# Optimization experiments

Hardware: AMD Instinct MI355X
Metric: run time of the kernel (lower is better)

Reference implementation:

```python
import jax, jax.numpy as jnp
from jax import lax
import numpy as np

DN = ('NCHW', 'OIHW', 'NCHW')
LEAKY_SLOPE = 0.01  # torch nn.LeakyReLU default


def conv(x, w, b=None, stride=1, pad=0):
    y = lax.conv_general_dilated(x, w, (stride, stride), [(pad, pad), (pad, pad)],
                                 dimension_numbers=DN)
    return y if b is None else y + b[None, :, None, None]


def conv_transpose2d(x, w, b):
    # torch ConvTranspose2d(k=4, s=2, p=1); w layout (Cin, Cout, 4, 4)
    wf = jnp.transpose(jnp.flip(w, (2, 3)), (1, 0, 2, 3))  # -> OIHW
    y = lax.conv_general_dilated(x, wf, (1, 1), [(2, 2), (2, 2)],
                                 lhs_dilation=(2, 2), dimension_numbers=DN)
    return y + b[None, :, None, None]


def residual_stack(x, rw3, rw1):
    # 6 ResidualLayers: x + conv1x1(relu(conv3x3(x))), both convs bias-free
    for i in range(rw3.shape[0]):
        h = jax.nn.relu(conv(x, rw3[i], pad=1))
        x = x + conv(h, rw1[i])
    return x


def vector_quantize(latents, codebook):
    # latents: [B, D, H, W] -> NHWC
    lat = jnp.transpose(latents, (0, 2, 3, 1))
    B, H, W, D = lat.shape
    flat = lat.reshape(-1, D)  # [N, D]
    # pairwise squared distances [N, K]
    dist = (jnp.sum(flat ** 2, axis=1, keepdims=True)
            + jnp.sum(codebook ** 2, axis=1)
            - 2.0 * flat @ codebook.T)
    inds = jnp.argmin(dist, axis=1)            # [N]
    q = codebook[inds].reshape(B, H, W, D)     # gather == one-hot matmul
    commitment_loss = jnp.mean((lax.stop_gradient(q) - lat) ** 2)
    embedding_loss = jnp.mean((q - lax.stop_gradient(lat)) ** 2)
    q_st = lat + lax.stop_gradient(q - lat)    # straight-through
    return jnp.transpose(q_st, (0, 3, 1, 2)), embedding_loss, commitment_loss


def setup_inputs() -> dict:
    key = jax.random.key(0)
    ks = iter(jax.random.split(key, 32))
    B, C, S = 16, 3, 128
    H0, H1 = 128, 256          # hidden_dims
    D, K = 64, 512             # embedding_dim, num_embeddings
    n_res = 6

    def w(shape, scale=0.05):
        return (jax.random.normal(next(ks), shape, dtype=jnp.float32) * scale)

    inp = {
        'x': jax.random.normal(next(ks), (B, C, S, S), dtype=jnp.float32),
        # encoder
        'ew0': w((H0, C, 4, 4)), 'eb0': jnp.zeros((H0,), jnp.float32),
        'ew1': w((H1, H0, 4, 4)), 'eb1': jnp.zeros((H1,), jnp.float32),
        'ew2': w((H1, H1, 3, 3)), 'eb2': jnp.zeros((H1,), jnp.float32),
        'erw3': w((n_res, H1, H1, 3, 3)),
        'erw1': w((n_res, H1, H1, 1, 1)),
        'ew3': w((D, H1, 1, 1)), 'eb3': jnp.zeros((D,), jnp.float32),
        # codebook, uniform(-1/K, 1/K) as in torch init
        'codebook': jax.random.uniform(next(ks), (K, D), jnp.float32, -1.0 / K, 1.0 / K),
        # decoder
        'dw0': w((H1, D, 3, 3)), 'db0': jnp.zeros((H1,), jnp.float32),
        'drw3': w((n_res, H1, H1, 3, 3)),
        'drw1': w((n_res, H1, H1, 1, 1)),
        'tw0': w((H1, H0, 4, 4)), 'tb0': jnp.zeros((H0,), jnp.float32),
        'tw1': w((H0, C, 4, 4)), 'tb1': jnp.zeros((C,), jnp.float32),
    }
    return inp


def reference(x, ew0, eb0, ew1, eb1, ew2, eb2, erw3, erw1, ew3, eb3,
              codebook, dw0, db0, drw3, drw1, tw0, tb0, tw1, tb1):
    lrelu = lambda t: jax.nn.leaky_relu(t, LEAKY_SLOPE)
    # encoder: two stride-2 downsamples, conv3x3, 6 residuals, 1x1 -> D
    h = lrelu(conv(x, ew0, eb0, stride=2, pad=1))   # [B,128,64,64]
    h = lrelu(conv(h, ew1, eb1, stride=2, pad=1))   # [B,256,32,32]
    h = lrelu(conv(h, ew2, eb2, stride=1, pad=1))
    h = residual_stack(h, erw3, erw1)
    h = lrelu(h)
    z = lrelu(conv(h, ew3, eb3))                    # [B,64,32,32]
    # vector quantization
    q, embedding_loss, commitment_loss = vector_quantize(z, codebook)
    # decoder
    d = lrelu(conv(q, dw0, db0, stride=1, pad=1))   # [B,256,32,32]
    d = residual_stack(d, drw3, drw1)
    d = lrelu(d)
    d = lrelu(conv_transpose2d(d, tw0, tb0))        # [B,128,64,64]
    recons = jnp.tanh(conv_transpose2d(d, tw1, tb1))  # [B,3,128,128]
    return recons, embedding_loss, commitment_loss
```

## Files before the change

### kernel.cpp

```cpp
#include <hip/hip_runtime.h>
#include <math.h>


typedef __attribute__((ext_vector_type(8))) short bf16x8;
typedef __attribute__((ext_vector_type(4))) float f32x4;

__device__ __forceinline__ float bf2f(short s) {
    unsigned u = ((unsigned)(unsigned short)s) << 16;
    return __builtin_bit_cast(float, u);
}
__device__ __forceinline__ unsigned short f2bfu(float f) {
    unsigned u = __builtin_bit_cast(unsigned, f);
    u = (u + 0x7fff + ((u >> 16) & 1)) >> 16;
    return (unsigned short)u;
}
__device__ __forceinline__ short f2bf(float f) { return (short)f2bfu(f); }
__device__ __forceinline__ int pack2(float a, float b) {
    return (int)f2bfu(a) | ((int)f2bfu(b) << 16);
}

template<int ACT>
__device__ __forceinline__ float actf(float v) {
    if (ACT == 1) return fmaxf(v, 0.f);
    if (ACT == 2) return v > 0.f ? v : 0.01f * v;
    return v;
}

__device__ __forceinline__ void gload_lds16(const void* g, void* l) {
    __builtin_amdgcn_global_load_lds(
        (const __attribute__((address_space(1))) unsigned int*)g,
        (__attribute__((address_space(3))) unsigned int*)l, 16, 0, 0);
}

__device__ __forceinline__ int fof(int r) { return (r & 3) ^ ((r >> 2) & 3); }

#define WAITV(N) asm volatile("s_waitcnt vmcnt(" #N ")" ::: "memory")

__device__ __forceinline__ void perm_one(const float* src, short* dst,
        int COUT, int CIN, int T, int i, int total) {
    if (i >= total) return;
    int ic = i % CIN; int r = i / CIN;
    int oc = r % COUT; r /= COUT;
    int t = r % T; int c = r / T;
    dst[i] = f2bf(src[(((size_t)c * COUT + oc) * CIN + ic) * T + t]);
}

__global__ __launch_bounds__(256) void prep_all_k(
        const float* ew1, const float* ew2, const float* erw3,
        const float* erw1, const float* ew3, const float* dw0,
        const float* drw3, const float* drw1, const float* tw0,
        short* Wp1, short* We2, short* Wer3, short* We11, short* Wz,
        short* Wd0, short* Wdr3, short* Wdr1, short* Wt0) {
    int bid = blockIdx.x, tid = threadIdx.x;
    if (bid < 2048) {
        perm_one(ew1, Wp1, 256, 128, 16, bid * 256 + tid, 524288);
    } else if (bid < 4352) {
        perm_one(ew2, We2, 256, 256, 9, (bid - 2048) * 256 + tid, 589824);
    } else if (bid < 18176) {
        perm_one(erw3, Wer3, 256, 256, 9, (bid - 4352) * 256 + tid, 3538944);
    } else if (bid < 19712) {
        perm_one(erw1, We11, 256, 256, 1, (bid - 18176) * 256 + tid, 393216);
    } else if (bid < 19776) {
        perm_one(ew3, Wz, 64, 256, 1, (bid - 19712) * 256 + tid, 16384);
    } else if (bid < 20352) {
        perm_one(dw0, Wd0, 256, 64, 9, (bid - 19776) * 256 + tid, 147456);
    } else if (bid < 34176) {
        perm_one(drw3, Wdr3, 256, 256, 9, (bid - 20352) * 256 + tid, 3538944);
    } else if (bid < 35712) {
        perm_one(drw1, Wdr1, 256, 256, 1, (bid - 34176) * 256 + tid, 393216);
    } else {
        int i = (bid - 35712) * 256 + tid;
        if (i < 524288) {
            int ic = i & 255; int r = i >> 8;
            int oc = r & 127; r >>= 7;
            int tap = r & 3; int par = r >> 2;
            int py = par >> 1, px = par & 1, my = tap >> 1, mx = tap & 1;
            int ky = 2 * my + (py ^ 1), kx = 2 * mx + (px ^ 1);
            Wt0[i] = f2bf(tw0[(((size_t)ic * 128 + oc) * 4 + ky) * 4 + kx]);
        }
    }
}

__global__ __launch_bounds__(256) void halo_zero_k(short* __restrict__ p,
        int W, int C) {
    int row = blockIdx.x, img = blockIdx.y;
    short* base = p + ((size_t)img * W + row) * W * C;
    bool full = (row < 2) || (row >= W - 2);
    int n = full ? W * C : 4 * C;
    for (int t = threadIdx.x * 8; t < n; t += 256 * 8) {
        int off = t;
        if (!full) off = (t < 2 * C) ? t : (W - 2) * C + (t - 2 * C);
        *(int4*)(base + off) = int4{0, 0, 0, 0};
    }
}

template<int CIN, int NTAPS, int TAPPAT, int SM, int INW, int OUTACT,
         bool HASB, bool FUSE>
__global__ __launch_bounds__(512, 1) void rconv_k(
        const short* __restrict__ in, const short* __restrict__ Wp,
        const float* __restrict__ bias, const short* __restrict__ W1p,
        short* __restrict__ outp) {
    constexpr int CH64 = (CIN >= 128) ? CIN / 64 : 1;
    constexpr int LG2 = (CH64 == 4) ? 2 : (CH64 == 2) ? 1 : 0;
    constexpr int ST = NTAPS * CH64;
    __shared__ short sLds[81920];
    const int tid = threadIdx.x;
    const int lane = tid & 63, wv = tid >> 6;
    const int wc = wv & 3, kg = wv >> 2;
    const int pix0 = blockIdx.x * 64;
    const int l15 = lane & 15, hi = lane >> 4;
    const int sl = (hi ^ fof(l15)) * 8;

    const int arow = (tid >> 2) & 63, akk = tid >> 8, aslot = tid & 3;
    const short* Aptr;
    {
        int pixa = pix0 + arow;
        int ba = pixa >> 10, Ya = (pixa >> 5) & 31, Xa = pixa & 31;
        Aptr = in + (size_t)((ba * INW + SM * Ya + 2) * INW + (SM * Xa + 2)) * CIN
                  + akk * 32 + (aslot ^ fof(arow)) * 8;
    }
    const short* Bptr[4];
#pragma unroll
    for (int j = 0; j < 4; j++) {
        int gb = tid + 512 * j;
        int kkb = gb >> 10, oc = (gb >> 2) & 255, slb = gb & 3;
        Bptr[j] = Wp + (size_t)oc * CIN + kkb * 32 + ((slb ^ fof(oc)) * 8);
    }

    auto stage = [&](int s, int bi) {
        int t = s >> LG2;
        int c0 = (s & (CH64 - 1)) * 64;
        int rof, cof;
        if (TAPPAT == 1) { rof = t / 3 - 1; cof = t % 3 - 1; }
        else             { rof = (t >> 2) - 1; cof = (t & 3) - 1; }
        int aoff = (rof * INW + cof) * CIN + c0;
        int woff = t * (256 * CIN) + c0;
        char* L = (char*)sLds + bi * 40960;
        gload_lds16(Aptr + aoff, L + tid * 16);
#pragma unroll
        for (int j = 0; j < 4; j++)
            gload_lds16(Bptr[j] + woff, L + 8192 + (tid + 512 * j) * 16);
    };

    f32x4 acc[4][4];
#pragma unroll
    for (int mi = 0; mi < 4; mi++)
#pragma unroll
        for (int ni = 0; ni < 4; ni++) acc[mi][ni] = f32x4{0.f, 0.f, 0.f, 0.f};

    stage(0, 0);
    stage(1, 1);
    stage(2, 2);
    int bi = 0;
    for (int s = 0; s < ST; ++s) {
        if (s < ST - 2)      { WAITV(10); }
        else if (s == ST - 2){ WAITV(5); }
        else                 { WAITV(0); }
        __builtin_amdgcn_s_barrier();
        if (s + 3 < ST) stage(s + 3, (bi + 3) & 3);
        const short* LA = sLds + bi * 20480 + kg * 2048;
        const short* LB = sLds + bi * 20480 + 4096 + kg * 8192;
        bf16x8 af[4], bfr[4];
#pragma unroll
        for (int mi = 0; mi < 4; mi++)
            af[mi] = *(const bf16x8*)(LA + (mi * 16 + l15) * 32 + sl);
#pragma unroll
        for (int ni = 0; ni < 4; ni++)
            bfr[ni] = *(const bf16x8*)(LB + (wc * 64 + ni * 16 + l15) * 32 + sl);
        __builtin_amdgcn_s_setprio(1);
#pragma unroll
        for (int mi = 0; mi < 4; mi++)
#pragma unroll
            for (int ni = 0; ni < 4; ni++)
                acc[mi][ni] = __builtin_amdgcn_mfma_f32_16x16x32_bf16(
                    af[mi], bfr[ni], acc[mi][ni], 0, 0, 0);
        __builtin_amdgcn_s_setprio(0);
        bi = (bi + 1) & 3;
    }

    float* MB = (float*)sLds;

    const short* W1ptr[4];
    if (FUSE) {
#pragma unroll
        for (int j = 0; j < 4; j++) {
            int gb = tid + 512 * j;
            int kkb = gb >> 10, oc = (gb >> 2) & 255, slb = gb & 3;
            W1ptr[j] = W1p + (size_t)oc * 256 + kkb * 32 + ((slb ^ fof(oc)) * 8);
        }
    }
    auto stage2 = [&](int c) {
        char* L = (char*)sLds + 98304 + (c & 1) * 32768;
#pragma unroll
        for (int j = 0; j < 4; j++)
            gload_lds16(W1ptr[j] + c * 64, L + (tid + 512 * j) * 16);
    };

    __syncthreads();
    if (FUSE) { stage2(0); stage2(1); }
    if (kg == 1) {
#pragma unroll
        for (int mi = 0; mi < 4; mi++)
#pragma unroll
            for (int ni = 0; ni < 4; ni++)
#pragma unroll
                for (int r = 0; r < 4; r++)
                    MB[(mi * 16 + hi * 4 + r) * 256 + wc * 64 + ni * 16 + l15]
                        = acc[mi][ni][r];
    }
    __syncthreads();

    if (!FUSE) {
        if (kg == 0) {
#pragma unroll
            for (int mi = 0; mi < 4; mi++)
#pragma unroll
                for (int ni = 0; ni < 4; ni++) {
                    int col = wc * 64 + ni * 16 + l15;
                    float b = HASB ? bias[col] : 0.f;
#pragma unroll
                    for (int r = 0; r < 4; r++) {
                        int row = mi * 16 + hi * 4 + r;
                        MB[row * 256 + col] += acc[mi][ni][r] + b;
                    }
                }
        }
        __syncthreads();
#pragma unroll
        for (int j = 0; j < 4; j++) {
            int idx = j * 512 + tid;
            int p = idx >> 5, c0 = (idx & 31) * 8;
            int pix = pix0 + p;
            int b = pix >> 10, Y = (pix >> 5) & 31, X = pix & 31;
            size_t base = (((size_t)b * 36 + Y + 2) * 36 + X + 2) * 256 + c0;
            const float4* m4 = (const float4*)(MB + idx * 8);
            float4 lo = m4[0], hv = m4[1];
            int pk[4];
            pk[0] = pack2(actf<OUTACT>(lo.x), actf<OUTACT>(lo.y));
            pk[1] = pack2(actf<OUTACT>(lo.z), actf<OUTACT>(lo.w));
            pk[2] = pack2(actf<OUTACT>(hv.x), actf<OUTACT>(hv.y));
            pk[3] = pack2(actf<OUTACT>(hv.z), actf<OUTACT>(hv.w));
            *(int4*)(outp + base) = *(int4*)pk;
        }
        return;
    }

    short* H = sLds + 32768;
    if (kg == 0) {
#pragma unroll
        for (int mi = 0; mi < 4; mi++)
#pragma unroll
            for (int ni = 0; ni < 4; ni++) {
                int col = wc * 64 + ni * 16 + l15;
#pragma unroll
                for (int r = 0; r < 4; r++) {
                    int row = mi * 16 + hi * 4 + r;
                    float v = acc[mi][ni][r] + MB[row * 256 + col];
                    H[((col >> 5) * 64 + row) * 32
                      + (((col >> 3) & 3) ^ fof(row)) * 8 + (col & 7)]
                        = f2bf(fmaxf(v, 0.f));
                }
            }
    }
    __syncthreads();

    f32x4 acc2[4][4];
#pragma unroll
    for (int mi = 0; mi < 4; mi++)
#pragma unroll
        for (int ni = 0; ni < 4; ni++) acc2[mi][ni] = f32x4{0.f, 0.f, 0.f, 0.f};

    for (int s2 = 0; s2 < 4; ++s2) {
        if (s2 < 3) { WAITV(4); } else { WAITV(0); }
        __builtin_amdgcn_s_barrier();
        const short* HB = H + (s2 * 2 + kg) * 2048;
        const short* LW = sLds + 49152 + (s2 & 1) * 16384 + kg * 8192;
        bf16x8 af2[4], bf2r[4];
#pragma unroll
        for (int mi = 0; mi < 4; mi++)
            af2[mi] = *(const bf16x8*)(HB + (mi * 16 + l15) * 32 + sl);
#pragma unroll
        for (int ni = 0; ni < 4; ni++)
            bf2r[ni] = *(const bf16x8*)(LW + (wc * 64 + ni * 16 + l15) * 32 + sl);
        asm volatile("s_waitcnt lgkmcnt(0)" ::: "memory");
        __builtin_amdgcn_sched_barrier(0);
        __builtin_amdgcn_s_barrier();
        if (s2 < 2) stage2(s2 + 2);
        __builtin_amdgcn_s_setprio(1);
#pragma unroll
        for (int mi = 0; mi < 4; mi++)
#pragma unroll
            for (int ni = 0; ni < 4; ni++)
                acc2[mi][ni] = __builtin_amdgcn_mfma_f32_16x16x32_bf16(
                    af2[mi], bf2r[ni], acc2[mi][ni], 0, 0, 0);
        __builtin_amdgcn_s_setprio(0);
    }

    __syncthreads();
    if (kg == 1) {
#pragma unroll
        for (int mi = 0; mi < 4; mi++)
#pragma unroll
            for (int ni = 0; ni < 4; ni++)
#pragma unroll
                for (int r = 0; r < 4; r++)
                    MB[(mi * 16 + hi * 4 + r) * 256 + wc * 64 + ni * 16 + l15]
                        = acc2[mi][ni][r];
    }
    __syncthreads();
    if (kg == 0) {
#pragma unroll
        for (int mi = 0; mi < 4; mi++)
#pragma unroll
            for (int ni = 0; ni < 4; ni++) {
                int col = wc * 64 + ni * 16 + l15;
#pragma unroll
                for (int r = 0; r < 4; r++) {
                    int row = mi * 16 + hi * 4 + r;
                    MB[row * 256 + col] += acc2[mi][ni][r];
                }
            }
    }
    __syncthreads();
#pragma unroll
    for (int j = 0; j < 4; j++) {
        int idx = j * 512 + tid;
        int p = idx >> 5, c0 = (idx & 31) * 8;
        int pix = pix0 + p;
        int b = pix >> 10, Y = (pix >> 5) & 31, X = pix & 31;
        size_t base = (((size_t)b * 36 + Y + 2) * 36 + X + 2) * 256 + c0;
        const float4* m4 = (const float4*)(MB + idx * 8);
        float4 lo = m4[0], hv = m4[1];
        bf16x8 rv = *(const bf16x8*)(in + base);
        int pk[4];
        pk[0] = pack2(actf<OUTACT>(lo.x + bf2f(rv[0])),
                      actf<OUTACT>(lo.y + bf2f(rv[1])));
        pk[1] = pack2(actf<OUTACT>(lo.z + bf2f(rv[2])),
                      actf<OUTACT>(lo.w + bf2f(rv[3])));
        pk[2] = pack2(actf<OUTACT>(hv.x + bf2f(rv[4])),
                      actf<OUTACT>(hv.y + bf2f(rv[5])));
        pk[3] = pack2(actf<OUTACT>(hv.z + bf2f(rv[6])),
                      actf<OUTACT>(hv.w + bf2f(rv[7])));
        *(int4*)(outp + base) = *(int4*)pk;
    }
}

template<int CIN, int COUT, int NTAPS, int TAPPAT, int SM, int INW,
         int OUTACT, bool RES, bool HASB, int OUTMODE, int BN>
__global__ __launch_bounds__(256) void gconv_k(
        const short* __restrict__ in, const short* __restrict__ Wp,
        const float* __restrict__ bias, const short* __restrict__ res,
        void* __restrict__ outp) {
    constexpr int KCH = CIN / 32;
    constexpr int LG = (KCH == 8) ? 3 : (KCH == 4) ? 2 : (KCH == 2) ? 1 : 0;
    constexpr int ST = NTAPS * KCH;
    constexpr int NF = BN / 32;
    constexpr int WN = BN / 2;
    __shared__ short sA[3 * 128 * 32];
    __shared__ short sB[3 * BN * 32];
    const int tid = threadIdx.x;
    const int lane = tid & 63, wv = tid >> 6;
    const int wr = wv >> 1, wc = wv & 1;
    const int pix0 = blockIdx.x * 128;
    const int oc0 = blockIdx.y * BN;
    int py = 0, px = 0;
    if (TAPPAT == 3) {
        int par = blockIdx.z;
        py = par >> 1; px = par & 1;
        Wp += (size_t)par * NTAPS * COUT * CIN;
    }
    const int sp = tid >> 2;
    const int swz = ((tid & 3) ^ fof(sp)) * 8;
    int rbA[2];
#pragma unroll
    for (int rd = 0; rd < 2; rd++) {
        int pix = pix0 + sp + rd * 64;
        int b = pix >> 10, Y = (pix >> 5) & 31, X = pix & 31;
        rbA[rd] = ((b * INW + SM * Y + 2) * INW + (SM * X + 2)) * CIN + swz;
    }
    const int wb0 = (oc0 + sp) * CIN + swz;
    const int wb1 = (oc0 + sp + 64) * CIN + swz;

    f32x4 acc[4][NF];
#pragma unroll
    for (int i = 0; i < 4; i++)
#pragma unroll
        for (int j = 0; j < NF; j++) acc[i][j] = f32x4{0.f, 0.f, 0.f, 0.f};

    const int sslot = ((lane >> 4) ^ fof(lane & 15)) * 8;
    const int abase = (wr * 64 + (lane & 15)) * 32 + sslot;
    const int bbase = (wc * WN + (lane & 15)) * 32 + sslot;

    auto stage = [&](int s, int biq) {
        int t = s >> LG, c = s & (KCH - 1);
        int rof, cof;
        if (TAPPAT == 0) { rof = 0; cof = 0; }
        else if (TAPPAT == 1) { rof = t / 3 - 1; cof = t % 3 - 1; }
        else if (TAPPAT == 2) { rof = t / 4 - 1; cof = t % 4 - 1; }
        else { int my = t >> 1, mx = t & 1;
               rof = (py == 0) ? -my : 1 - my;
               cof = (px == 0) ? -mx : 1 - mx; }
        const int tapoff = (rof * INW + cof) * CIN + c * 32;
        char* a = (char*)sA + biq * 8192;
        char* b = (char*)sB + biq * (BN * 64);
        const short* wt = Wp + (size_t)t * COUT * CIN + c * 32;
        gload_lds16(in + rbA[0] + tapoff, a + tid * 16);
        gload_lds16(in + rbA[1] + tapoff, a + 4096 + tid * 16);
        gload_lds16(wt + wb0, b + tid * 16);
        if (BN == 128) gload_lds16(wt + wb1, b + 4096 + tid * 16);
    };

    stage(0, 0);
    stage(1, 1);
    int cur = 0;
    for (int s = 0; s < ST; ++s) {
        if (s < ST - 1) {
            if (BN == 128) { WAITV(4); } else { WAITV(3); }
        } else {
            WAITV(0);
        }
        __builtin_amdgcn_s_barrier();
        int nxt = cur + 2; if (nxt >= 3) nxt -= 3;
        if (s + 2 < ST) stage(s + 2, nxt);
        const short* a = sA + cur * 4096;
        const short* b = sB + cur * (BN * 32);
        bf16x8 af[4], bfm[NF];
#pragma unroll
        for (int mi = 0; mi < 4; mi++)
            af[mi] = *(const bf16x8*)(a + abase + mi * 512);
#pragma unroll
        for (int ni = 0; ni < NF; ni++)
            bfm[ni] = *(const bf16x8*)(b + bbase + ni * 512);
        __builtin_amdgcn_s_setprio(1);
#pragma unroll
        for (int mi = 0; mi < 4; mi++)
#pragma unroll
            for (int ni = 0; ni < NF; ni++)
                acc[mi][ni] = __builtin_amdgcn_mfma_f32_16x16x32_bf16(
                    af[mi], bfm[ni], acc[mi][ni], 0, 0, 0);
        __builtin_amdgcn_s_setprio(0);
        cur = (cur == 2) ? 0 : cur + 1;
    }
#pragma unroll
    for (int mi = 0; mi < 4; mi++) {
#pragma unroll
        for (int r = 0; r < 4; r++) {
            int pix = pix0 + wr * 64 + mi * 16 + (lane >> 4) * 4 + r;
            int b = pix >> 10, Y = (pix >> 5) & 31, X = pix & 31;
            size_t rowoff = 0;
            if (OUTMODE == 0)
                rowoff = (((size_t)b * 36 + Y + 2) * 36 + X + 2) * COUT;
            else if (OUTMODE == 2)
                rowoff = (((size_t)b * 68 + 2 * Y + py + 2) * 68 + 2 * X + px + 2) * 128;
#pragma unroll
            for (int ni = 0; ni < NF; ni++) {
                int col = oc0 + wc * WN + ni * 16 + (lane & 15);
                float v = acc[mi][ni][r];
                if (HASB) v += bias[col];
                if (OUTMODE == 1) {
                    ((float*)outp)[(size_t)pix * COUT + col] = actf<OUTACT>(v);
                } else {
                    size_t off = rowoff + col;
                    if (RES) v += bf2f(res[off]);
                    ((short*)outp)[off] = f2bf(actf<OUTACT>(v));
                }
            }
        }
    }
}

__global__ __launch_bounds__(256) void conv0_k(const float* __restrict__ x,
        const float* __restrict__ W, const float* __restrict__ bias,
        short* __restrict__ P0) {
    __shared__ float sIn[3 * 4 * 130];
    __shared__ float sW[48 * 4 * 36];
    int y = blockIdx.x, b = blockIdx.y;
    int tid = threadIdx.x;
    for (int t = tid; t < 6144; t += 256) {
        int k = t >> 7, oc = t & 127;
        sW[(k * 4 + (oc >> 5)) * 36 + (oc & 31)] = W[(size_t)oc * 48 + k];
    }
    for (int t = tid; t < 1560; t += 256) {
        int ic = t / 520; int rem = t - ic * 520;
        int ry = rem / 130, rx = rem - ry * 130;
        int iy = 2 * y - 1 + ry, ix = rx - 1;
        float v = 0.f;
        if ((unsigned)iy < 128u && (unsigned)ix < 128u)
            v = x[((size_t)b * 3 + ic) * 16384 + iy * 128 + ix];
        sIn[t] = v;
    }
    __syncthreads();
    int p = tid >> 2, g = tid & 3, oc0 = g * 32;
    float acc[32];
#pragma unroll
    for (int o = 0; o < 32; o++) acc[o] = bias[oc0 + o];
#pragma unroll
    for (int ic = 0; ic < 3; ic++)
#pragma unroll
        for (int ky = 0; ky < 4; ky++) {
            const float* ib = sIn + ic * 520 + ky * 130 + 2 * p;
#pragma unroll
            for (int kx = 0; kx < 4; kx++) {
                float xv = ib[kx];
                const float* wr_ = sW + ((ic * 16 + ky * 4 + kx) * 4 + g) * 36;
#pragma unroll
                for (int q = 0; q < 8; q++) {
                    float4 w = *(const float4*)(wr_ + q * 4);
                    acc[4 * q + 0] += w.x * xv; acc[4 * q + 1] += w.y * xv;
                    acc[4 * q + 2] += w.z * xv; acc[4 * q + 3] += w.w * xv;
                }
            }
        }
    size_t base = (((size_t)b * 68 + y + 2) * 68 + p + 2) * 128 + oc0;
#pragma unroll
    for (int q4 = 0; q4 < 4; q4++) {
        int pk[4];
#pragma unroll
        for (int j = 0; j < 4; j++) {
            float v0 = actf<2>(acc[q4 * 8 + 2 * j]);
            float v1 = actf<2>(acc[q4 * 8 + 2 * j + 1]);
            pk[j] = pack2(v0, v1);
        }
        *(int4*)(P0 + base + q4 * 8) = *(int4*)pk;
    }
}

__global__ __launch_bounds__(256) void vq_argmin_k(const float* __restrict__ zr,
        const float* __restrict__ cb, int* __restrict__ ind) {
    __shared__ short sZ[2][128 * 32];
    __shared__ short sC[2][128 * 32];
    __shared__ float sN[128];
    const int tid = threadIdx.x;
    const int lane = tid & 63, wv = tid >> 6;
    const int pos0 = blockIdx.x * 128;
#pragma unroll
    for (int it = 0; it < 4; ++it) {
        int task = tid + it * 256;
        int row = task >> 3, kq = task & 7;
        const float4* zp = (const float4*)(zr + (size_t)(pos0 + row) * 64 + kq * 8);
        float4 v0 = zp[0], v1 = zp[1];
        int slot = ((kq & 3) ^ fof(row)) * 8;
        short tmp[8] = {f2bf(v0.x), f2bf(v0.y), f2bf(v0.z), f2bf(v0.w),
                        f2bf(v1.x), f2bf(v1.y), f2bf(v1.z), f2bf(v1.w)};
        *(bf16x8*)&sZ[kq >> 2][row * 32 + slot] = *(bf16x8*)tmp;
    }
    const int sslot = ((lane >> 4) ^ fof(lane & 15)) * 8;
    const int l15 = lane & 15;
    float best[2][4]; int bidx[2][4];
#pragma unroll
    for (int mi = 0; mi < 2; mi++)
#pragma unroll
        for (int r = 0; r < 4; r++) { best[mi][r] = INFINITY; bidx[mi][r] = 0; }
    for (int ch = 0; ch < 4; ++ch) {
        __syncthreads();
#pragma unroll
        for (int it = 0; it < 4; ++it) {
            int task = tid + it * 256;
            int row = task >> 3, kq = task & 7;
            const float4* cp = (const float4*)(cb + (size_t)(ch * 128 + row) * 64 + kq * 8);
            float4 v0 = cp[0], v1 = cp[1];
            int slot = ((kq & 3) ^ fof(row)) * 8;
            short tmp[8] = {f2bf(v0.x), f2bf(v0.y), f2bf(v0.z), f2bf(v0.w),
                            f2bf(v1.x), f2bf(v1.y), f2bf(v1.z), f2bf(v1.w)};
            *(bf16x8*)&sC[kq >> 2][row * 32 + slot] = *(bf16x8*)tmp;
        }
        if (tid < 128) {
            const float4* cp = (const float4*)(cb + (size_t)(ch * 128 + tid) * 64);
            float s = 0.f;
#pragma unroll
            for (int q = 0; q < 16; q++) {
                float4 v = cp[q];
                s += v.x * v.x + v.y * v.y + v.z * v.z + v.w * v.w;
            }
            sN[tid] = s;
        }
        __syncthreads();
        f32x4 acc[2][8];
#pragma unroll
        for (int mi = 0; mi < 2; mi++)
#pragma unroll
            for (int ni = 0; ni < 8; ni++) acc[mi][ni] = f32x4{0.f, 0.f, 0.f, 0.f};
#pragma unroll
        for (int kc = 0; kc < 2; ++kc) {
            bf16x8 za[2], ca[8];
#pragma unroll
            for (int mi = 0; mi < 2; mi++)
                za[mi] = *(const bf16x8*)&sZ[kc][(wv * 32 + mi * 16 + l15) * 32 + sslot];
#pragma unroll
            for (int ni = 0; ni < 8; ni++)
                ca[ni] = *(const bf16x8*)&sC[kc][(ni * 16 + l15) * 32 + sslot];
#pragma unroll
            for (int mi = 0; mi < 2; mi++)
#pragma unroll
                for (int ni = 0; ni < 8; ni++)
                    acc[mi][ni] = __builtin_amdgcn_mfma_f32_16x16x32_bf16(
                        za[mi], ca[ni], acc[mi][ni], 0, 0, 0);
        }
#pragma unroll
        for (int mi = 0; mi < 2; mi++)
#pragma unroll
            for (int ni = 0; ni < 8; ni++) {
                float nrm = sN[ni * 16 + l15];
                int idx = ch * 128 + ni * 16 + l15;
#pragma unroll
                for (int r = 0; r < 4; r++) {
                    float sc = nrm - 2.f * acc[mi][ni][r];
                    if (sc < best[mi][r]) { best[mi][r] = sc; bidx[mi][r] = idx; }
                }
            }
    }
#pragma unroll
    for (int m = 1; m < 16; m <<= 1) {
#pragma unroll
        for (int mi = 0; mi < 2; mi++)
#pragma unroll
            for (int r = 0; r < 4; r++) {
                float os = __shfl_xor(best[mi][r], m);
                int   oi = __shfl_xor(bidx[mi][r], m);
                if (os < best[mi][r] || (os == best[mi][r] && oi < bidx[mi][r])) {
                    best[mi][r] = os; bidx[mi][r] = oi;
                }
            }
    }
    if (l15 == 0) {
        int g = lane >> 4;
#pragma unroll
        for (int mi = 0; mi < 2; mi++)
#pragma unroll
            for (int r = 0; r < 4; r++)
                ind[pos0 + wv * 32 + mi * 16 + g * 4 + r] = bidx[mi][r];
    }
}

__global__ __launch_bounds__(256) void vq_gather_k(const float* __restrict__ zr,
        const float* __restrict__ cb, const int* __restrict__ ind,
        short* __restrict__ q, float* __restrict__ part) {
    int pos = blockIdx.x * 256 + threadIdx.x;
    int b = pos >> 10, hw = pos & 1023, y = hw >> 5, xx = hw & 31;
    int idx = ind[pos];
    const float4* cp = (const float4*)(cb + (size_t)idx * 64);
    const float4* zp = (const float4*)(zr + (size_t)pos * 64);
    size_t qb = (((size_t)b * 36 + y + 2) * 36 + xx + 2) * 64;
    float sum = 0.f;
#pragma unroll
    for (int d4 = 0; d4 < 16; d4++) {
        float4 c = cp[d4], z = zp[d4];
        float dx = c.x - z.x, dy = c.y - z.y, dz = c.z - z.z, dw = c.w - z.w;
        sum += dx * dx + dy * dy + dz * dz + dw * dw;
        ((int*)(q + qb))[2 * d4] = pack2(c.x, c.y);
        ((int*)(q + qb))[2 * d4 + 1] = pack2(c.z, c.w);
    }
#pragma unroll
    for (int m = 1; m < 64; m <<= 1) sum += __shfl_xor(sum, m);
    __shared__ float sred[4];
    int lane = threadIdx.x & 63, wvv = threadIdx.x >> 6;
    if (lane == 0) sred[wvv] = sum;
    __syncthreads();
    if (threadIdx.x == 0)
        part[blockIdx.x] = sred[0] + sred[1] + sred[2] + sred[3];
}

__global__ void finalize_k(const float* __restrict__ part, float* __restrict__ out) {
    if (threadIdx.x == 0) {
        float s = 0.f;
        for (int k = 0; k < 64; k++) s += part[k];
        float m = s / 1048576.f;
        out[786432] = m;
        out[786433] = m;
    }
}

__global__ __launch_bounds__(256) void tw1_k(const short* __restrict__ in,
        const float* __restrict__ W, const float* __restrict__ bias,
        float* __restrict__ out) {
    __shared__ float sW[16 * 128 * 4];
    int b = blockIdx.y, y0 = blockIdx.x * 8;
    int tid = threadIdx.x;
    for (int t = tid; t < 2048; t += 256) {
        int k = t >> 7, ic = t & 127;
        float4 v;
        v.x = W[((size_t)ic * 3 + 0) * 16 + k];
        v.y = W[((size_t)ic * 3 + 1) * 16 + k];
        v.z = W[((size_t)ic * 3 + 2) * 16 + k];
        v.w = 0.f;
        *(float4*)&sW[t * 4] = v;
    }
    __syncthreads();
    int r = tid >> 5, g = tid & 31;
    int oy = y0 + r, py = oy & 1, Y = oy >> 1, pxp = g & 1;
    float acc[4][3];
#pragma unroll
    for (int p = 0; p < 4; p++)
#pragma unroll
        for (int o = 0; o < 3; o++) acc[p][o] = 0.f;
#pragma unroll
    for (int my = 0; my < 2; my++) {
        int iy = Y + ((py == 0) ? -my : 1 - my) + 2;
        const short* rowp = in + (((size_t)b * 68 + iy) * 68) * 128;
        int ky = 2 * my + (py ^ 1);
#pragma unroll
        for (int mx = 0; mx < 2; mx++) {
            int kx = 2 * mx + (pxp ^ 1);
            int cof = ((pxp == 0) ? -mx : 1 - mx) + 2;
            const float* wbase = &sW[((ky * 4 + kx) * 128) * 4];
            const short* pptr[4];
#pragma unroll
            for (int p = 0; p < 4; p++) {
                int X = ((g + 32 * p) >> 1) + cof;
                pptr[p] = rowp + (size_t)X * 128;
            }
            for (int icb = 0; icb < 16; icb++) {
                bf16x8 v[4];
#pragma unroll
                for (int p = 0; p < 4; p++)
                    v[p] = *(const bf16x8*)(pptr[p] + icb * 8);
#pragma unroll
                for (int j = 0; j < 8; j++) {
                    float4 w = *(const float4*)&wbase[(icb * 8 + j) * 4];
#pragma unroll
                    for (int p = 0; p < 4; p++) {
                        float xv = bf2f(v[p][j]);
                        acc[p][0] += w.x * xv;
                        acc[p][1] += w.y * xv;
                        acc[p][2] += w.z * xv;
                    }
                }
            }
        }
    }
#pragma unroll
    for (int p = 0; p < 4; p++) {
        int ox = g + 32 * p;
#pragma unroll
        for (int o = 0; o < 3; o++)
            out[(((size_t)b * 3 + o) << 14) + oy * 128 + ox] =
                tanhf(acc[p][o] + bias[o]);
    }
}

extern "C" void kernel_launch(void* const* d_in, const int* in_sizes, int n_in,
                              void* d_out, int out_size, void* d_ws, size_t ws_size,
                              hipStream_t stream) {
    const float* x    = (const float*)d_in[0];
    const float* ew0  = (const float*)d_in[1];
    const float* eb0  = (const float*)d_in[2];
    const float* ew1  = (const float*)d_in[3];
    const float* eb1  = (const float*)d_in[4];
    const float* ew2  = (const float*)d_in[5];
    const float* eb2  = (const float*)d_in[6];
    const float* erw3 = (const float*)d_in[7];
    const float* erw1 = (const float*)d_in[8];
    const float* ew3  = (const float*)d_in[9];
    const float* eb3  = (const float*)d_in[10];
    const float* cbk  = (const float*)d_in[11];
    const float* dw0  = (const float*)d_in[12];
    const float* db0  = (const float*)d_in[13];
    const float* drw3 = (const float*)d_in[14];
    const float* drw1 = (const float*)d_in[15];
    const float* tw0  = (const float*)d_in[16];
    const float* tb0  = (const float*)d_in[17];
    const float* tw1  = (const float*)d_in[18];
    const float* tb1  = (const float*)d_in[19];
    float* out = (float*)d_out;

    short* S = (short*)d_ws;
    short* P0  = S;
    short* PB  = P0 + 9469952;
    short* PC  = PB + 5308416;
    short* Pq  = PC + 5308416;
    short* Wp1 = Pq + 1327104;
    short* We2 = Wp1 + 524288;
    short* Wer3 = We2 + 589824;
    short* We11 = Wer3 + 3538944;
    short* Wz   = We11 + 393216;
    short* Wd0  = Wz + 16384;
    short* Wdr3 = Wd0 + 147456;
    short* Wdr1 = Wdr3 + 3538944;
    short* Wt0  = Wdr1 + 393216;
    float* F   = (float*)(S + 31080448);
    float* Zr  = F;
    float* PART = Zr + 1048576;
    int*   IND = (int*)(PART + 64);

    halo_zero_k<<<dim3(68, 16), 256, 0, stream>>>(P0, 68, 128);
    halo_zero_k<<<dim3(36, 16), 256, 0, stream>>>(PB, 36, 256);
    halo_zero_k<<<dim3(36, 16), 256, 0, stream>>>(PC, 36, 256);
    halo_zero_k<<<dim3(36, 16), 256, 0, stream>>>(Pq, 36, 64);

    prep_all_k<<<37760, 256, 0, stream>>>(ew1, ew2, erw3, erw1, ew3, dw0,
        drw3, drw1, tw0, Wp1, We2, Wer3, We11, Wz, Wd0, Wdr3, Wdr1, Wt0);

    conv0_k<<<dim3(64, 16), 256, 0, stream>>>(x, ew0, eb0, P0);
    rconv_k<128, 16, 2, 2, 68, 2, true, false>
        <<<256, 512, 0, stream>>>(P0, Wp1, eb1, nullptr, PB);
    rconv_k<256, 9, 1, 1, 36, 2, true, false>
        <<<256, 512, 0, stream>>>(PB, We2, eb2, nullptr, PC);
    for (int i = 0; i < 6; i++) {
        short* inb  = (i & 1) ? PB : PC;
        short* outb = (i & 1) ? PC : PB;
        if (i < 5)
            rconv_k<256, 9, 1, 1, 36, 0, false, true>
                <<<256, 512, 0, stream>>>(inb, Wer3 + (size_t)i * 589824,
                    nullptr, We11 + (size_t)i * 65536, outb);
        else
            rconv_k<256, 9, 1, 1, 36, 2, false, true>
                <<<256, 512, 0, stream>>>(inb, Wer3 + (size_t)i * 589824,
                    nullptr, We11 + (size_t)i * 65536, outb);
    }
    gconv_k<256, 64, 1, 0, 1, 36, 2, false, true, 1, 64>
        <<<dim3(128, 1), 256, 0, stream>>>(PC, Wz, eb3, nullptr, Zr);

    vq_argmin_k<<<128, 256, 0, stream>>>(Zr, cbk, IND);
    vq_gather_k<<<64, 256, 0, stream>>>(Zr, cbk, IND, Pq, PART);

    rconv_k<64, 9, 1, 1, 36, 2, true, false>
        <<<256, 512, 0, stream>>>(Pq, Wd0, db0, nullptr, PC);
    for (int i = 0; i < 6; i++) {
        short* inb  = (i & 1) ? PB : PC;
        short* outb = (i & 1) ? PC : PB;
        if (i < 5)
            rconv_k<256, 9, 1, 1, 36, 0, false, true>
                <<<256, 512, 0, stream>>>(inb, Wdr3 + (size_t)i * 589824,
                    nullptr, Wdr1 + (size_t)i * 65536, outb);
        else
            rconv_k<256, 9, 1, 1, 36, 2, false, true>
                <<<256, 512, 0, stream>>>(inb, Wdr3 + (size_t)i * 589824,
                    nullptr, Wdr1 + (size_t)i * 65536, outb);
    }
    gconv_k<256, 128, 4, 3, 1, 36, 2, false, true, 2, 128>
        <<<dim3(128, 1, 4), 256, 0, stream>>>(PC, Wt0, tb0, nullptr, P0);
    tw1_k<<<dim3(16, 16), 256, 0, stream>>>(P0, tw1, tb1, out);

    finalize_k<<<1, 64, 0, stream>>>(PART, out);
}
```

Measured before the change: 621.3 us.

## Widen residual conv blocks to 1024 threads, MFMA conv0, merge halo kernels

The main fused conv kernel now runs 16 waves per block instead of 8, splitting the 64-pixel tile across two M-halves so each wave keeps half the accumulators. The prefetch pipeline drops from a 4-buffer, 3-ahead scheme to a 3-buffer, 2-ahead scheme. Separately, the first stride-2 conv is rewritten to use bf16 MFMA instead of scalar FP32 FMAs, and the four halo-zeroing launches are merged into one kernel. These changes aim to raise latency hiding and cut per-wave register pressure and launch overhead, at the cost of a shallower prefetch pipeline and more synchronisation per block.

```diff
diff --git a/kernel.cpp b/kernel.cpp
--- a/kernel.cpp
+++ b/kernel.cpp
@@ -35,6 +35,7 @@
 __device__ __forceinline__ int fof(int r) { return (r & 3) ^ ((r >> 2) & 3); }
 
 #define WAITV(N) asm volatile("s_waitcnt vmcnt(" #N ")" ::: "memory")
+#define LGKM0 asm volatile("s_waitcnt lgkmcnt(0)" ::: "memory")
 
 __device__ __forceinline__ void perm_one(const float* src, short* dst,
         int COUT, int CIN, int T, int i, int total) {
@@ -81,22 +82,34 @@
     }
 }
 
-__global__ __launch_bounds__(256) void halo_zero_k(short* __restrict__ p,
-        int W, int C) {
-    int row = blockIdx.x, img = blockIdx.y;
-    short* base = p + ((size_t)img * W + row) * W * C;
-    bool full = (row < 2) || (row >= W - 2);
-    int n = full ? W * C : 4 * C;
-    for (int t = threadIdx.x * 8; t < n; t += 256 * 8) {
-        int off = t;
-        if (!full) off = (t < 2 * C) ? t : (W - 2) * C + (t - 2 * C);
-        *(int4*)(base + off) = int4{0, 0, 0, 0};
-    }
+__global__ __launch_bounds__(256) void halo_all_k(short* P0, short* PB,
+        short* PC, short* Pq) {
+    int g = blockIdx.x * 256 + threadIdx.x;
+    short* base; int W, C, idx;
+    if (g < 135168)      { base = P0; W = 68; C = 128; idx = g; }
+    else if (g < 274432) { base = PB; W = 36; C = 256; idx = g - 135168; }
+    else if (g < 413696) { base = PC; W = 36; C = 256; idx = g - 274432; }
+    else                 { base = Pq; W = 36; C = 64;  idx = g - 413696; }
+    int c8 = C >> 3;
+    int per_img = (4 * W + (W - 4) * 4) * c8;
+    int img = idx / per_img, r = idx - img * per_img;
+    int row, off;
+    if (r < 4 * W * c8) {
+        int rr = r / (W * c8);
+        row = (rr < 2) ? rr : W - 4 + rr;
+        off = r - rr * (W * c8);
+    } else {
+        int r2 = r - 4 * W * c8;
+        row = 2 + r2 / (4 * c8);
+        int q = r2 - (row - 2) * (4 * c8);
+        off = (q < 2 * c8) ? q : (W - 2) * c8 + (q - 2 * c8);
+    }
+    ((int4*)(base + ((size_t)img * W + row) * W * C))[off] = int4{0, 0, 0, 0};
 }
 
 template<int CIN, int NTAPS, int TAPPAT, int SM, int INW, int OUTACT,
          bool HASB, bool FUSE>
-__global__ __launch_bounds__(512, 1) void rconv_k(
+__global__ __launch_bounds__(1024, 1) void rconv_k(
         const short* __restrict__ in, const short* __restrict__ Wp,
         const float* __restrict__ bias, const short* __restrict__ W1p,
         short* __restrict__ outp) {
@@ -106,23 +119,24 @@
     __shared__ short sLds[81920];
     const int tid = threadIdx.x;
     const int lane = tid & 63, wv = tid >> 6;
-    const int wc = wv & 3, kg = wv >> 2;
+    const int wc = wv & 3, mh = (wv >> 2) & 1, kg = wv >> 3;
     const int pix0 = blockIdx.x * 64;
     const int l15 = lane & 15, hi = lane >> 4;
-    const int sl = (hi ^ fof(l15)) * 8;
-
-    const int arow = (tid >> 2) & 63, akk = tid >> 8, aslot = tid & 3;
-    const short* Aptr;
-    {
+    const int sl = hi ^ fof(l15);
+    const bool low = (tid < 512);
+
+    const short* Aptr = in;
+    if (low) {
+        int arow = tid >> 3, aslot = tid & 7;
         int pixa = pix0 + arow;
         int ba = pixa >> 10, Ya = (pixa >> 5) & 31, Xa = pixa & 31;
         Aptr = in + (size_t)((ba * INW + SM * Ya + 2) * INW + (SM * Xa + 2)) * CIN
-                  + akk * 32 + (aslot ^ fof(arow)) * 8;
-    }
-    const short* Bptr[4];
-#pragma unroll
-    for (int j = 0; j < 4; j++) {
-        int gb = tid + 512 * j;
+             + (aslot >> 2) * 32 + (((aslot & 3) ^ fof(arow)) * 8);
+    }
+    const short* Bptr[2];
+#pragma unroll
+    for (int j = 0; j < 2; j++) {
+        int gb = tid + 1024 * j;
         int kkb = gb >> 10, oc = (gb >> 2) & 255, slb = gb & 3;
         Bptr[j] = Wp + (size_t)oc * CIN + kkb * 32 + ((slb ^ fof(oc)) * 8);
     }
@@ -133,107 +147,90 @@
         int rof, cof;
         if (TAPPAT == 1) { rof = t / 3 - 1; cof = t % 3 - 1; }
         else             { rof = (t >> 2) - 1; cof = (t & 3) - 1; }
-        int aoff = (rof * INW + cof) * CIN + c0;
+        char* L = (char*)sLds + bi * 40960;
+        if (low)
+            gload_lds16(Aptr + (rof * INW + cof) * CIN + c0, L + tid * 16);
         int woff = t * (256 * CIN) + c0;
-        char* L = (char*)sLds + bi * 40960;
-        gload_lds16(Aptr + aoff, L + tid * 16);
-#pragma unroll
-        for (int j = 0; j < 4; j++)
-            gload_lds16(Bptr[j] + woff, L + 8192 + (tid + 512 * j) * 16);
+        gload_lds16(Bptr[0] + woff, L + 8192 + tid * 16);
+        gload_lds16(Bptr[1] + woff, L + 8192 + (tid + 1024) * 16);
     };
 
-    f32x4 acc[4][4];
-#pragma unroll
-    for (int mi = 0; mi < 4; mi++)
+    f32x4 acc[2][4];
+#pragma unroll
+    for (int mi = 0; mi < 2; mi++)
 #pragma unroll
         for (int ni = 0; ni < 4; ni++) acc[mi][ni] = f32x4{0.f, 0.f, 0.f, 0.f};
 
     stage(0, 0);
     stage(1, 1);
-    stage(2, 2);
     int bi = 0;
     for (int s = 0; s < ST; ++s) {
-        if (s < ST - 2)      { WAITV(10); }
-        else if (s == ST - 2){ WAITV(5); }
-        else                 { WAITV(0); }
+        if (s < ST - 1) { if (low) { WAITV(3); } else { WAITV(2); } }
+        else { WAITV(0); }
         __builtin_amdgcn_s_barrier();
-        if (s + 3 < ST) stage(s + 3, (bi + 3) & 3);
-        const short* LA = sLds + bi * 20480 + kg * 2048;
-        const short* LB = sLds + bi * 20480 + 4096 + kg * 8192;
-        bf16x8 af[4], bfr[4];
-#pragma unroll
-        for (int mi = 0; mi < 4; mi++)
-            af[mi] = *(const bf16x8*)(LA + (mi * 16 + l15) * 32 + sl);
+        int nx = bi + 2; if (nx >= 3) nx -= 3;
+        if (s + 2 < ST) stage(s + 2, nx);
+        const short* LA = sLds + bi * 20480;
+        const short* LB = LA + 4096;
+        bf16x8 af[2], bfr[4];
+#pragma unroll
+        for (int mi = 0; mi < 2; mi++)
+            af[mi] = *(const bf16x8*)(LA + (mh * 32 + mi * 16 + l15) * 64
+                                      + kg * 32 + sl * 8);
 #pragma unroll
         for (int ni = 0; ni < 4; ni++)
-            bfr[ni] = *(const bf16x8*)(LB + (wc * 64 + ni * 16 + l15) * 32 + sl);
+            bfr[ni] = *(const bf16x8*)(LB + kg * 8192
+                                       + (wc * 64 + ni * 16 + l15) * 32 + sl * 8);
         __builtin_amdgcn_s_setprio(1);
 #pragma unroll
-        for (int mi = 0; mi < 4; mi++)
+        for (int mi = 0; mi < 2; mi++)
 #pragma unroll
             for (int ni = 0; ni < 4; ni++)
                 acc[mi][ni] = __builtin_amdgcn_mfma_f32_16x16x32_bf16(
                     af[mi], bfr[ni], acc[mi][ni], 0, 0, 0);
         __builtin_amdgcn_s_setprio(0);
-        bi = (bi + 1) & 3;
+        bi = (bi == 2) ? 0 : bi + 1;
     }
 
     float* MB = (float*)sLds;
 
-    const short* W1ptr[4];
-    if (FUSE) {
-#pragma unroll
-        for (int j = 0; j < 4; j++) {
-            int gb = tid + 512 * j;
-            int kkb = gb >> 10, oc = (gb >> 2) & 255, slb = gb & 3;
-            W1ptr[j] = W1p + (size_t)oc * 256 + kkb * 32 + ((slb ^ fof(oc)) * 8);
-        }
-    }
-    auto stage2 = [&](int c) {
-        char* L = (char*)sLds + 98304 + (c & 1) * 32768;
-#pragma unroll
-        for (int j = 0; j < 4; j++)
-            gload_lds16(W1ptr[j] + c * 64, L + (tid + 512 * j) * 16);
-    };
-
     __syncthreads();
-    if (FUSE) { stage2(0); stage2(1); }
     if (kg == 1) {
 #pragma unroll
-        for (int mi = 0; mi < 4; mi++)
+        for (int mi = 0; mi < 2; mi++)
 #pragma unroll
             for (int ni = 0; ni < 4; ni++)
 #pragma unroll
                 for (int r = 0; r < 4; r++)
-                    MB[(mi * 16 + hi * 4 + r) * 256 + wc * 64 + ni * 16 + l15]
-                        = acc[mi][ni][r];
+                    MB[(mh * 32 + mi * 16 + hi * 4 + r) * 256
+                       + wc * 64 + ni * 16 + l15] = acc[mi][ni][r];
     }
     __syncthreads();
 
     if (!FUSE) {
         if (kg == 0) {
 #pragma unroll
-            for (int mi = 0; mi < 4; mi++)
+            for (int mi = 0; mi < 2; mi++)
 #pragma unroll
                 for (int ni = 0; ni < 4; ni++) {
                     int col = wc * 64 + ni * 16 + l15;
                     float b = HASB ? bias[col] : 0.f;
 #pragma unroll
                     for (int r = 0; r < 4; r++) {
-                        int row = mi * 16 + hi * 4 + r;
+                        int row = mh * 32 + mi * 16 + hi * 4 + r;
                         MB[row * 256 + col] += acc[mi][ni][r] + b;
                     }
                 }
         }
         __syncthreads();
 #pragma unroll
-        for (int j = 0; j < 4; j++) {
-            int idx = j * 512 + tid;
+        for (int j = 0; j < 2; j++) {
+            int idx = j * 1024 + tid;
             int p = idx >> 5, c0 = (idx & 31) * 8;
             int pix = pix0 + p;
             int b = pix >> 10, Y = (pix >> 5) & 31, X = pix & 31;
             size_t base = (((size_t)b * 36 + Y + 2) * 36 + X + 2) * 256 + c0;
-            const float4* m4 = (const float4*)(MB + idx * 8);
+            const float4* m4 = (const float4*)(MB + p * 256 + c0);
             float4 lo = m4[0], hv = m4[1];
             int pk[4];
             pk[0] = pack2(actf<OUTACT>(lo.x), actf<OUTACT>(lo.y));
@@ -245,16 +242,31 @@
         return;
     }
 
+    const short* W1ptr[2];
+#pragma unroll
+    for (int j = 0; j < 2; j++) {
+        int gb = tid + 1024 * j;
+        int kkb = gb >> 10, oc = (gb >> 2) & 255, slb = gb & 3;
+        W1ptr[j] = W1p + (size_t)oc * 256 + kkb * 32 + ((slb ^ fof(oc)) * 8);
+    }
+    auto stage2 = [&](int c) {
+        char* L = (char*)sLds + 98304 + (c & 1) * 32768;
+        gload_lds16(W1ptr[0] + c * 64, L + tid * 16);
+        gload_lds16(W1ptr[1] + c * 64, L + (tid + 1024) * 16);
+    };
+    stage2(0);
+    stage2(1);
+
     short* H = sLds + 32768;
     if (kg == 0) {
 #pragma unroll
-        for (int mi = 0; mi < 4; mi++)
+        for (int mi = 0; mi < 2; mi++)
 #pragma unroll
             for (int ni = 0; ni < 4; ni++) {
                 int col = wc * 64 + ni * 16 + l15;
 #pragma unroll
                 for (int r = 0; r < 4; r++) {
-                    int row = mi * 16 + hi * 4 + r;
+                    int row = mh * 32 + mi * 16 + hi * 4 + r;
                     float v = acc[mi][ni][r] + MB[row * 256 + col];
                     H[((col >> 5) * 64 + row) * 32
                       + (((col >> 3) & 3) ^ fof(row)) * 8 + (col & 7)]
@@ -262,33 +274,39 @@
                 }
             }
     }
-    __syncthreads();
-
-    f32x4 acc2[4][4];
-#pragma unroll
-    for (int mi = 0; mi < 4; mi++)
+    LGKM0;
+    __builtin_amdgcn_sched_barrier(0);
+    __builtin_amdgcn_s_barrier();
+
+    f32x4 acc2[2][4];
+#pragma unroll
+    for (int mi = 0; mi < 2; mi++)
 #pragma unroll
         for (int ni = 0; ni < 4; ni++) acc2[mi][ni] = f32x4{0.f, 0.f, 0.f, 0.f};
 
     for (int s2 = 0; s2 < 4; ++s2) {
-        if (s2 < 3) { WAITV(4); } else { WAITV(0); }
+        if (s2 < 3) { WAITV(2); } else { WAITV(0); }
         __builtin_amdgcn_s_barrier();
-        const short* HB = H + (s2 * 2 + kg) * 2048;
+        int c = s2 * 2 + kg;
         const short* LW = sLds + 49152 + (s2 & 1) * 16384 + kg * 8192;
-        bf16x8 af2[4], bf2r[4];
-#pragma unroll
-        for (int mi = 0; mi < 4; mi++)
-            af2[mi] = *(const bf16x8*)(HB + (mi * 16 + l15) * 32 + sl);
+        bf16x8 af2[2], bf2r[4];
+#pragma unroll
+        for (int mi = 0; mi < 2; mi++) {
+            int row = mh * 32 + mi * 16 + l15;
+            af2[mi] = *(const bf16x8*)(H + (c * 64 + row) * 32
+                                       + (hi ^ fof(row)) * 8);
+        }
 #pragma unroll
         for (int ni = 0; ni < 4; ni++)
-            bf2r[ni] = *(const bf16x8*)(LW + (wc * 64 + ni * 16 + l15) * 32 + sl);
-        asm volatile("s_waitcnt lgkmcnt(0)" ::: "memory");
+            bf2r[ni] = *(const bf16x8*)(LW + (wc * 64 + ni * 16 + l15) * 32
+                                        + sl * 8);
+        LGKM0;
         __builtin_amdgcn_sched_barrier(0);
         __builtin_amdgcn_s_barrier();
         if (s2 < 2) stage2(s2 + 2);
         __builtin_amdgcn_s_setprio(1);
 #pragma unroll
-        for (int mi = 0; mi < 4; mi++)
+        for (int mi = 0; mi < 2; mi++)
 #pragma unroll
             for (int ni = 0; ni < 4; ni++)
                 acc2[mi][ni] = __builtin_amdgcn_mfma_f32_16x16x32_bf16(
@@ -299,37 +317,37 @@
     __syncthreads();
     if (kg == 1) {
 #pragma unroll
-        for (int mi = 0; mi < 4; mi++)
+        for (int mi = 0; mi < 2; mi++)
 #pragma unroll
             for (int ni = 0; ni < 4; ni++)
 #pragma unroll
                 for (int r = 0; r < 4; r++)
-                    MB[(mi * 16 + hi * 4 + r) * 256 + wc * 64 + ni * 16 + l15]
-                        = acc2[mi][ni][r];
+                    MB[(mh * 32 + mi * 16 + hi * 4 + r) * 256
+                       + wc * 64 + ni * 16 + l15] = acc2[mi][ni][r];
     }
     __syncthreads();
     if (kg == 0) {
 #pragma unroll
-        for (int mi = 0; mi < 4; mi++)
+        for (int mi = 0; mi < 2; mi++)
 #pragma unroll
             for (int ni = 0; ni < 4; ni++) {
                 int col = wc * 64 + ni * 16 + l15;
 #pragma unroll
                 for (int r = 0; r < 4; r++) {
-                    int row = mi * 16 + hi * 4 + r;
+                    int row = mh * 32 + mi * 16 + hi * 4 + r;
                     MB[row * 256 + col] += acc2[mi][ni][r];
                 }
             }
     }
     __syncthreads();
 #pragma unroll
-    for (int j = 0; j < 4; j++) {
-        int idx = j * 512 + tid;
+    for (int j = 0; j < 2; j++) {
+        int idx = j * 1024 + tid;
         int p = idx >> 5, c0 = (idx & 31) * 8;
         int pix = pix0 + p;
         int b = pix >> 10, Y = (pix >> 5) & 31, X = pix & 31;
         size_t base = (((size_t)b * 36 + Y + 2) * 36 + X + 2) * 256 + c0;
-        const float4* m4 = (const float4*)(MB + idx * 8);
+        const float4* m4 = (const float4*)(MB + p * 256 + c0);
         float4 lo = m4[0], hv = m4[1];
         bf16x8 rv = *(const bf16x8*)(in + base);
         int pk[4];
@@ -472,56 +490,78 @@
 __global__ __launch_bounds__(256) void conv0_k(const float* __restrict__ x,
         const float* __restrict__ W, const float* __restrict__ bias,
         short* __restrict__ P0) {
-    __shared__ float sIn[3 * 4 * 130];
-    __shared__ float sW[48 * 4 * 36];
+    __shared__ float sP[3 * 4 * 132];
+    __shared__ short sB[8192];
+    __shared__ float sMB[8192];
     int y = blockIdx.x, b = blockIdx.y;
     int tid = threadIdx.x;
-    for (int t = tid; t < 6144; t += 256) {
-        int k = t >> 7, oc = t & 127;
-        sW[(k * 4 + (oc >> 5)) * 36 + (oc & 31)] = W[(size_t)oc * 48 + k];
+    int lane = tid & 63, w = tid >> 6;
+    int l15 = lane & 15, hi = lane >> 4;
+    int sl = hi ^ fof(l15);
+    for (int t = tid; t < 8192; t += 256) {
+        int oc = t >> 6, k = t & 63;
+        float v = (k < 48) ? W[(size_t)oc * 48 + k] : 0.f;
+        int kk = k >> 5, slot = (k >> 3) & 3, j = k & 7;
+        sB[oc * 64 + kk * 32 + ((slot ^ fof(oc)) * 8) + j] = f2bf(v);
     }
     for (int t = tid; t < 1560; t += 256) {
-        int ic = t / 520; int rem = t - ic * 520;
-        int ry = rem / 130, rx = rem - ry * 130;
+        int ic = t / 520; int r = t - ic * 520;
+        int ry = r / 130, rx = r - ry * 130;
         int iy = 2 * y - 1 + ry, ix = rx - 1;
         float v = 0.f;
         if ((unsigned)iy < 128u && (unsigned)ix < 128u)
             v = x[((size_t)b * 3 + ic) * 16384 + iy * 128 + ix];
-        sIn[t] = v;
+        sP[(ic * 4 + ry) * 132 + rx] = v;
     }
     __syncthreads();
-    int p = tid >> 2, g = tid & 3, oc0 = g * 32;
-    float acc[32];
-#pragma unroll
-    for (int o = 0; o < 32; o++) acc[o] = bias[oc0 + o];
-#pragma unroll
-    for (int ic = 0; ic < 3; ic++)
-#pragma unroll
-        for (int ky = 0; ky < 4; ky++) {
-            const float* ib = sIn + ic * 520 + ky * 130 + 2 * p;
-#pragma unroll
-            for (int kx = 0; kx < 4; kx++) {
-                float xv = ib[kx];
-                const float* wr_ = sW + ((ic * 16 + ky * 4 + kx) * 4 + g) * 36;
-#pragma unroll
-                for (int q = 0; q < 8; q++) {
-                    float4 w = *(const float4*)(wr_ + q * 4);
-                    acc[4 * q + 0] += w.x * xv; acc[4 * q + 1] += w.y * xv;
-                    acc[4 * q + 2] += w.z * xv; acc[4 * q + 3] += w.w * xv;
-                }
+    int ox = w * 16 + l15;
+    bf16x8 af[2];
+#pragma unroll
+    for (int kk = 0; kk < 2; kk++) {
+        short tmp[8];
+#pragma unroll
+        for (int j = 0; j < 8; j++) {
+            int k = kk * 32 + hi * 8 + j;
+            float v = 0.f;
+            if (k < 48) {
+                int ic = k >> 4, ky = (k >> 2) & 3, kx = k & 3;
+                v = sP[(ic * 4 + ky) * 132 + 2 * ox + kx];
             }
-        }
-    size_t base = (((size_t)b * 68 + y + 2) * 68 + p + 2) * 128 + oc0;
-#pragma unroll
-    for (int q4 = 0; q4 < 4; q4++) {
+            tmp[j] = f2bf(v);
+        }
+        af[kk] = *(bf16x8*)tmp;
+    }
+    f32x4 acc[8];
+#pragma unroll
+    for (int ni = 0; ni < 8; ni++) acc[ni] = f32x4{0.f, 0.f, 0.f, 0.f};
+#pragma unroll
+    for (int ni = 0; ni < 8; ni++) {
+        int oc = ni * 16 + l15;
+        bf16x8 b0 = *(const bf16x8*)(sB + oc * 64 + sl * 8);
+        bf16x8 b1 = *(const bf16x8*)(sB + oc * 64 + 32 + sl * 8);
+        acc[ni] = __builtin_amdgcn_mfma_f32_16x16x32_bf16(af[0], b0, acc[ni], 0, 0, 0);
+        acc[ni] = __builtin_amdgcn_mfma_f32_16x16x32_bf16(af[1], b1, acc[ni], 0, 0, 0);
+    }
+#pragma unroll
+    for (int ni = 0; ni < 8; ni++) {
+        int col = ni * 16 + l15;
+        float bv = bias[col];
+#pragma unroll
+        for (int r = 0; r < 4; r++)
+            sMB[(w * 16 + hi * 4 + r) * 128 + col] = actf<2>(acc[ni][r] + bv);
+    }
+    __syncthreads();
+#pragma unroll
+    for (int it = 0; it < 4; it++) {
+        int idx = it * 256 + tid;
+        int p = idx >> 4, c0 = (idx & 15) * 8;
+        size_t base = (((size_t)b * 68 + y + 2) * 68 + p + 2) * 128 + c0;
+        const float4* m4 = (const float4*)(sMB + p * 128 + c0);
+        float4 lo = m4[0], hv = m4[1];
         int pk[4];
-#pragma unroll
-        for (int j = 0; j < 4; j++) {
-            float v0 = actf<2>(acc[q4 * 8 + 2 * j]);
-            float v1 = actf<2>(acc[q4 * 8 + 2 * j + 1]);
-            pk[j] = pack2(v0, v1);
-        }
-        *(int4*)(P0 + base + q4 * 8) = *(int4*)pk;
+        pk[0] = pack2(lo.x, lo.y); pk[1] = pack2(lo.z, lo.w);
+        pk[2] = pack2(hv.x, hv.y); pk[3] = pack2(hv.z, hv.w);
+        *(int4*)(P0 + base) = *(int4*)pk;
     }
 }
 
@@ -782,29 +822,25 @@
     float* PART = Zr + 1048576;
     int*   IND = (int*)(PART + 64);
 
-    halo_zero_k<<<dim3(68, 16), 256, 0, stream>>>(P0, 68, 128);
-    halo_zero_k<<<dim3(36, 16), 256, 0, stream>>>(PB, 36, 256);
-    halo_zero_k<<<dim3(36, 16), 256, 0, stream>>>(PC, 36, 256);
-    halo_zero_k<<<dim3(36, 16), 256, 0, stream>>>(Pq, 36, 64);
-
+    halo_all_k<<<1752, 256, 0, stream>>>(P0, PB, PC, Pq);
     prep_all_k<<<37760, 256, 0, stream>>>(ew1, ew2, erw3, erw1, ew3, dw0,
         drw3, drw1, tw0, Wp1, We2, Wer3, We11, Wz, Wd0, Wdr3, Wdr1, Wt0);
 
     conv0_k<<<dim3(64, 16), 256, 0, stream>>>(x, ew0, eb0, P0);
     rconv_k<128, 16, 2, 2, 68, 2, true, false>
-        <<<256, 512, 0, stream>>>(P0, Wp1, eb1, nullptr, PB);
+        <<<256, 1024, 0, stream>>>(P0, Wp1, eb1, nullptr, PB);
     rconv_k<256, 9, 1, 1, 36, 2, true, false>
-        <<<256, 512, 0, stream>>>(PB, We2, eb2, nullptr, PC);
+        <<<256, 1024, 0, stream>>>(PB, We2, eb2, nullptr, PC);
     for (int i = 0; i < 6; i++) {
         short* inb  = (i & 1) ? PB : PC;
         short* outb = (i & 1) ? PC : PB;
         if (i < 5)
             rconv_k<256, 9, 1, 1, 36, 0, false, true>
-                <<<256, 512, 0, stream>>>(inb, Wer3 + (size_t)i * 589824,
+                <<<256, 1024, 0, stream>>>(inb, Wer3 + (size_t)i * 589824,
                     nullptr, We11 + (size_t)i * 65536, outb);
         else
             rconv_k<256, 9, 1, 1, 36, 2, false, true>
-                <<<256, 512, 0, stream>>>(inb, Wer3 + (size_t)i * 589824,
+                <<<256, 1024, 0, stream>>>(inb, Wer3 + (size_t)i * 589824,
                     nullptr, We11 + (size_t)i * 65536, outb);
     }
     gconv_k<256, 64, 1, 0, 1, 36, 2, false, true, 1, 64>
@@ -814,17 +850,17 @@
     vq_gather_k<<<64, 256, 0, stream>>>(Zr, cbk, IND, Pq, PART);
 
     rconv_k<64, 9, 1, 1, 36, 2, true, false>
-        <<<256, 512, 0, stream>>>(Pq, Wd0, db0, nullptr, PC);
+        <<<256, 1024, 0, stream>>>(Pq, Wd0, db0, nullptr, PC);
     for (int i = 0; i < 6; i++) {
         short* inb  = (i & 1) ? PB : PC;
         short* outb = (i & 1) ? PC : PB;
         if (i < 5)
             rconv_k<256, 9, 1, 1, 36, 0, false, true>
-                <<<256, 512, 0, stream>>>(inb, Wdr3 + (size_t)i * 589824,
+                <<<256, 1024, 0, stream>>>(inb, Wdr3 + (size_t)i * 589824,
                     nullptr, Wdr1 + (size_t)i * 65536, outb);
         else
             rconv_k<256, 9, 1, 1, 36, 2, false, true>
-                <<<256, 512, 0, stream>>>(inb, Wdr3 + (size_t)i * 589824,
+                <<<256, 1024, 0, stream>>>(inb, Wdr3 + (size_t)i * 589824,
                     nullptr, Wdr1 + (size_t)i * 65536, outb);
     }
     gconv_k<256, 128, 4, 3, 1, 36, 2, false, true, 2, 128>
```

New measurement: 595.1 us. 1.04x faster.
